# Kernel optimization log

Hardware: AMD Instinct MI355X
Metric: run time of the kernel (lower is better)

Reference implementation:

```python
import jax, jax.numpy as jnp
import numpy as np

N, P1, P2, D = 4, 8192, 8192, 3
BIG = 1e10  # masks out padded target points before top-k (pytorch3d uses +inf)


def setup_inputs() -> dict:
    key = jax.random.key(0)
    k1, k2, k3 = jax.random.split(key, 3)
    pred_points = jax.random.normal(k1, (N, P1, D), dtype=jnp.float32)
    target_points = jax.random.normal(k2, (N, P2, D), dtype=jnp.float32)
    # ragged target lengths in [P2//2, P2] (always > 0 so every batch element is 'visible')
    target_lengths = jax.random.randint(k3, (N,), P2 // 2, P2 + 1, dtype=jnp.int32)
    return {
        "pred_points": pred_points,
        "target_points": target_points,
        "target_lengths": target_lengths,
        "num_neighbours": 1,
    }


def reference(pred_points, target_points, target_lengths, num_neighbours):
    x, y = pred_points, target_points  # [N,P1,D], [N,P2,D]
    n, p1, _ = x.shape
    p2 = y.shape[1]
    x2 = jnp.sum(x * x, axis=-1)
    y2 = jnp.sum(y * y, axis=-1)
    d2 = x2[:, :, None] + y2[:, None, :] - 2.0 * jnp.einsum('nid,njd->nij', x, y)
    d2 = jnp.maximum(d2, 0.0)

    # mask of invalid (padded) target points per batch: j >= target_lengths[b]
    y_pad = jnp.arange(p2)[None, :] >= target_lengths[:, None]  # [N,P2]

    # knn_points(x -> y): invalid y columns pushed to BIG before top-k smallest
    dxy = jnp.where(y_pad[:, None, :], BIG, d2)
    nn_x = -jax.lax.top_k(-dxy, num_neighbours)[0]          # [N,P1,K]
    cham_x = jnp.sum(jnp.mean(nn_x, axis=-1), axis=1) / p1  # point_reduction='mean'

    # knn_points(y -> x): all x points valid; zero out padded y rows afterwards
    dyx = jnp.swapaxes(d2, 1, 2)                            # [N,P2,P1]
    nn_y = -jax.lax.top_k(-dyx, num_neighbours)[0]          # [N,P2,K]
    cham_y_pts = jnp.where(y_pad, 0.0, jnp.mean(nn_y, axis=-1))
    cham_y = jnp.sum(cham_y_pts, axis=1) / target_lengths.astype(x.dtype)

    # batch_reduction='mean'
    loss = (jnp.sum(cham_x) + jnp.sum(cham_y)) / n
    return loss
```

## Files before the change

### kernel.cpp

```cpp
#include <hip/hip_runtime.h>

constexpr int N = 4;
constexpr int P = 8192;
constexpr int TILE = 256;
constexpr int MI = 8;
constexpr int ROWS = 256;
constexpr int RG = P / ROWS;

__global__ __launch_bounds__(256) void chamfer_min_kernel(
    const float* __restrict__ pred, const float* __restrict__ targ,
    const int* __restrict__ lens, float* __restrict__ ws)
{
    const int nseg = gridDim.y;
    const int segc = P / nseg;
    const int seg  = blockIdx.y;
    int id = blockIdx.x;
    const int rg  = id & (RG - 1); id >>= 5;
    const int b   = id & (N - 1);  id >>= 2;
    const int dir = id;
    const int row0 = rg * ROWS;
    const int c0   = seg * segc;
    const int L    = lens[b];
    const int tid  = threadIdx.x;
    const int chunk   = tid >> 5;
    const int rowtile = tid & 31;

    float* slot = ws + (((size_t)dir * N + b) * nseg + seg) * P + row0;

    if (dir == 1 && row0 >= L) return;
    if (dir == 0 && c0 >= L) {
        slot[tid] = 1e30f;
        return;
    }

    const float* rbase = (dir == 0 ? pred : targ) + (size_t)b * P * 3;
    const float* cbase = (dir == 0 ? targ : pred) + (size_t)b * P * 3;

    float rx[MI], ry[MI], rz[MI], best[MI];
    #pragma unroll
    for (int k = 0; k < MI; ++k) {
        const float* p = rbase + (size_t)(row0 + rowtile + 32 * k) * 3;
        rx[k] = p[0]; ry[k] = p[1]; rz[k] = p[2];
        best[k] = 1e30f;
    }

    __shared__ float4 sy[TILE];
    __shared__ float  red[ROWS * 9];

    int vc = segc;
    if (dir == 0 && L - c0 < segc) vc = L - c0;
    const int nt = (vc + TILE - 1) / TILE;

    for (int t = 0; t < nt; ++t) {
        const int col = c0 + t * TILE + tid;
        float4 cv;
        if (dir == 0 && col >= L) {
            cv = make_float4(0.f, 0.f, 0.f, 1e30f);
        } else {
            const float* p = cbase + (size_t)col * 3;
            const float a = p[0], bb = p[1], cc = p[2];
            cv = make_float4(-2.f*a, -2.f*bb, -2.f*cc, a*a + bb*bb + cc*cc);
        }
        __syncthreads();
        sy[tid] = cv;
        __syncthreads();

        const float4* sp = &sy[chunk * 32];
        #pragma unroll 4
        for (int jj = 0; jj < 32; jj += 2) {
            const float4 q0 = sp[jj];
            const float4 q1 = sp[jj + 1];
            #pragma unroll
            for (int k = 0; k < MI; ++k) {
                float d0 = fmaf(rx[k], q0.x, fmaf(ry[k], q0.y, fmaf(rz[k], q0.z, q0.w)));
                float d1 = fmaf(rx[k], q1.x, fmaf(ry[k], q1.y, fmaf(rz[k], q1.z, q1.w)));
                best[k] = fminf(best[k], fminf(d0, d1));
            }
        }
    }

    #pragma unroll
    for (int k = 0; k < MI; ++k)
        red[(rowtile + 32 * k) * 9 + chunk] = best[k];
    if (chunk == 0) {
        #pragma unroll
        for (int k = 0; k < MI; ++k)
            red[(rowtile + 32 * k) * 9 + 8] =
                fmaf(rx[k], rx[k], fmaf(ry[k], ry[k], rz[k] * rz[k]));
    }
    __syncthreads();

    {
        const float* r = &red[tid * 9];
        float v = fminf(fminf(fminf(r[0], r[1]), fminf(r[2], r[3])),
                        fminf(fminf(r[4], r[5]), fminf(r[6], r[7])));
        slot[tid] = v + r[8];
    }
}

__global__ __launch_bounds__(256) void chamfer_reduce_kernel(
    const float* __restrict__ ws, const int* __restrict__ lens,
    float* __restrict__ out, int nseg)
{
    const int item = blockIdx.x * 256 + threadIdx.x;
    const int dir = item >> 15;
    const int b   = (item >> 13) & (N - 1);
    const int p   = item & (P - 1);
    const int L   = lens[b];

    float c = 0.f;
    if (dir == 0 || p < L) {
        const float* base = ws + (((size_t)dir * N + b) * nseg) * P + p;
        float v = base[0];
        for (int s = 1; s < nseg; ++s) v = fminf(v, base[(size_t)s * P]);
        v = fmaxf(v, 0.f);
        c = dir ? v / ((float)L * (float)N) : v * (1.0f / ((float)P * (float)N));
    }
    #pragma unroll
    for (int off = 32; off; off >>= 1) c += __shfl_down(c, off, 64);
    __shared__ float acc[4];
    if ((threadIdx.x & 63) == 0) acc[threadIdx.x >> 6] = c;
    __syncthreads();
    if (threadIdx.x == 0) atomicAdd(out, acc[0] + acc[1] + acc[2] + acc[3]);
}

extern "C" void kernel_launch(void* const* d_in, const int* in_sizes, int n_in,
                              void* d_out, int out_size, void* d_ws, size_t ws_size,
                              hipStream_t stream)
{
    const float* pred = (const float*)d_in[0];
    const float* targ = (const float*)d_in[1];
    const int*   lens = (const int*)d_in[2];
    float* out = (float*)d_out;
    float* ws  = (float*)d_ws;

    const int nseg = (ws_size >= (size_t)2 * N * 16 * P * sizeof(float)) ? 16 : 8;

    hipMemsetAsync(out, 0, out_size * sizeof(float), stream);
    dim3 grid(2 * N * RG, nseg);
    chamfer_min_kernel<<<grid, 256, 0, stream>>>(pred, targ, lens, ws);
    chamfer_reduce_kernel<<<(2 * N * P) / 256, 256, 0, stream>>>(ws, lens, out, nseg);
}
```

Baseline: 105.2 us.

## Precompute transformed points and double-buffer column tiles via async global-to-LDS loads

Adds a prep kernel that writes every point once as a float4 (-2x,-2y,-2z,|p|^2), with padded targets given a large norm. The min kernel then streams column tiles straight into a double-buffered LDS array using global_load_lds, overlapping the next tile's load with compute and using one barrier per tile instead of two. The segment count is fixed at 8 rather than 16 when workspace allows, which halves the parallelism over columns. The change also adds an extra kernel launch and an extra pass over the inputs.

```diff
diff --git a/kernel.cpp b/kernel.cpp
--- a/kernel.cpp
+++ b/kernel.cpp
@@ -2,70 +2,82 @@
 
 constexpr int N = 4;
 constexpr int P = 8192;
+constexpr int NSEG = 8;
+constexpr int SEGC = P / NSEG;
 constexpr int TILE = 256;
 constexpr int MI = 8;
 constexpr int ROWS = 256;
 constexpr int RG = P / ROWS;
+constexpr size_t TRANS_F = (size_t)2 * N * P * 4;
+
+__global__ __launch_bounds__(256) void chamfer_prep_kernel(
+    const float* __restrict__ pred, const float* __restrict__ targ,
+    const int* __restrict__ lens, float4* __restrict__ trans)
+{
+    const int i = blockIdx.x * 256 + threadIdx.x;
+    const int side = i >> 15;
+    const int b    = (i >> 13) & (N - 1);
+    const int j    = i & (P - 1);
+    const float* s = (side ? targ : pred) + ((size_t)b * P + j) * 3;
+    const float x = s[0], y = s[1], z = s[2];
+    float w = fmaf(x, x, fmaf(y, y, z * z));
+    if (side == 1 && j >= lens[b]) w = 1e30f;
+    trans[i] = make_float4(-2.f * x, -2.f * y, -2.f * z, w);
+}
 
 __global__ __launch_bounds__(256) void chamfer_min_kernel(
-    const float* __restrict__ pred, const float* __restrict__ targ,
-    const int* __restrict__ lens, float* __restrict__ ws)
+    const int* __restrict__ lens, const float4* __restrict__ trans,
+    float* __restrict__ partial)
 {
-    const int nseg = gridDim.y;
-    const int segc = P / nseg;
-    const int seg  = blockIdx.y;
+    const int seg = blockIdx.y;
     int id = blockIdx.x;
     const int rg  = id & (RG - 1); id >>= 5;
     const int b   = id & (N - 1);  id >>= 2;
     const int dir = id;
     const int row0 = rg * ROWS;
-    const int c0   = seg * segc;
+    const int c0   = seg * SEGC;
     const int L    = lens[b];
     const int tid  = threadIdx.x;
     const int chunk   = tid >> 5;
     const int rowtile = tid & 31;
+    const int wave = tid >> 6, lane = tid & 63;
 
-    float* slot = ws + (((size_t)dir * N + b) * nseg + seg) * P + row0;
+    float* slot = partial + (((size_t)dir * N + b) * NSEG + seg) * P + row0;
+    if (dir == 1 && row0 >= L) return;
+    if (dir == 0 && c0 >= L) { slot[tid] = 1e30f; return; }
 
-    if (dir == 1 && row0 >= L) return;
-    if (dir == 0 && c0 >= L) {
-        slot[tid] = 1e30f;
-        return;
-    }
+    const float4* rsrc = trans + ((size_t)(dir == 0 ? 0 : 1) * N + b) * P;
+    const float4* csrc = trans + ((size_t)(dir == 0 ? 1 : 0) * N + b) * P;
 
-    const float* rbase = (dir == 0 ? pred : targ) + (size_t)b * P * 3;
-    const float* cbase = (dir == 0 ? targ : pred) + (size_t)b * P * 3;
-
-    float rx[MI], ry[MI], rz[MI], best[MI];
+    float rx[MI], ry[MI], rz[MI], rw[MI], best[MI];
     #pragma unroll
     for (int k = 0; k < MI; ++k) {
-        const float* p = rbase + (size_t)(row0 + rowtile + 32 * k) * 3;
-        rx[k] = p[0]; ry[k] = p[1]; rz[k] = p[2];
+        const float4 t = rsrc[row0 + rowtile + 32 * k];
+        rx[k] = -0.5f * t.x; ry[k] = -0.5f * t.y; rz[k] = -0.5f * t.z;
+        rw[k] = t.w;
         best[k] = 1e30f;
     }
 
-    __shared__ float4 sy[TILE];
+    __shared__ float4 buf[2][TILE];
     __shared__ float  red[ROWS * 9];
 
-    int vc = segc;
-    if (dir == 0 && L - c0 < segc) vc = L - c0;
+    int vc = SEGC;
+    if (dir == 0 && L - c0 < SEGC) vc = L - c0;
     const int nt = (vc + TILE - 1) / TILE;
 
+    __builtin_amdgcn_global_load_lds(
+        (const __attribute__((address_space(1))) void*)(csrc + c0 + wave * 64 + lane),
+        (__attribute__((address_space(3))) void*)&buf[0][wave * 64], 16, 0, 0);
+    __syncthreads();
+
     for (int t = 0; t < nt; ++t) {
-        const int col = c0 + t * TILE + tid;
-        float4 cv;
-        if (dir == 0 && col >= L) {
-            cv = make_float4(0.f, 0.f, 0.f, 1e30f);
-        } else {
-            const float* p = cbase + (size_t)col * 3;
-            const float a = p[0], bb = p[1], cc = p[2];
-            cv = make_float4(-2.f*a, -2.f*bb, -2.f*cc, a*a + bb*bb + cc*cc);
-        }
-        __syncthreads();
-        sy[tid] = cv;
-        __syncthreads();
+        const int cur = t & 1;
+        if (t + 1 < nt)
+            __builtin_amdgcn_global_load_lds(
+                (const __attribute__((address_space(1))) void*)(csrc + c0 + (t + 1) * TILE + wave * 64 + lane),
+                (__attribute__((address_space(3))) void*)&buf[cur ^ 1][wave * 64], 16, 0, 0);
 
-        const float4* sp = &sy[chunk * 32];
+        const float4* sp = &buf[cur][chunk * 32];
         #pragma unroll 4
         for (int jj = 0; jj < 32; jj += 2) {
             const float4 q0 = sp[jj];
@@ -77,6 +89,7 @@
                 best[k] = fminf(best[k], fminf(d0, d1));
             }
         }
+        __syncthreads();
     }
 
     #pragma unroll
@@ -85,8 +98,7 @@
     if (chunk == 0) {
         #pragma unroll
         for (int k = 0; k < MI; ++k)
-            red[(rowtile + 32 * k) * 9 + 8] =
-                fmaf(rx[k], rx[k], fmaf(ry[k], ry[k], rz[k] * rz[k]));
+            red[(rowtile + 32 * k) * 9 + 8] = rw[k];
     }
     __syncthreads();
 
@@ -99,8 +111,8 @@
 }
 
 __global__ __launch_bounds__(256) void chamfer_reduce_kernel(
-    const float* __restrict__ ws, const int* __restrict__ lens,
-    float* __restrict__ out, int nseg)
+    const float* __restrict__ partial, const int* __restrict__ lens,
+    float* __restrict__ out)
 {
     const int item = blockIdx.x * 256 + threadIdx.x;
     const int dir = item >> 15;
@@ -110,9 +122,10 @@
 
     float c = 0.f;
     if (dir == 0 || p < L) {
-        const float* base = ws + (((size_t)dir * N + b) * nseg) * P + p;
+        const float* base = partial + (((size_t)dir * N + b) * NSEG) * P + p;
         float v = base[0];
-        for (int s = 1; s < nseg; ++s) v = fminf(v, base[(size_t)s * P]);
+        #pragma unroll
+        for (int s = 1; s < NSEG; ++s) v = fminf(v, base[(size_t)s * P]);
         v = fmaxf(v, 0.f);
         c = dir ? v / ((float)L * (float)N) : v * (1.0f / ((float)P * (float)N));
     }
@@ -132,12 +145,12 @@
     const float* targ = (const float*)d_in[1];
     const int*   lens = (const int*)d_in[2];
     float* out = (float*)d_out;
-    float* ws  = (float*)d_ws;
-
-    const int nseg = (ws_size >= (size_t)2 * N * 16 * P * sizeof(float)) ? 16 : 8;
+    float4* trans   = (float4*)d_ws;
+    float*  partial = (float*)d_ws + TRANS_F;
 
     hipMemsetAsync(out, 0, out_size * sizeof(float), stream);
-    dim3 grid(2 * N * RG, nseg);
-    chamfer_min_kernel<<<grid, 256, 0, stream>>>(pred, targ, lens, ws);
-    chamfer_reduce_kernel<<<(2 * N * P) / 256, 256, 0, stream>>>(ws, lens, out, nseg);
+    chamfer_prep_kernel<<<(2 * N * P) / 256, 256, 0, stream>>>(pred, targ, lens, trans);
+    dim3 grid(2 * N * RG, NSEG);
+    chamfer_min_kernel<<<grid, 256, 0, stream>>>(lens, trans, partial);
+    chamfer_reduce_kernel<<<(2 * N * P) / 256, 256, 0, stream>>>(partial, lens, out);
 }
```

Result: no change. 105.5 us (+0.3%).
